# Optimization experiments

Hardware: AMD Instinct MI355X
Metric: run time of the kernel (lower is better)

## Reference

```python
import jax, jax.numpy as jnp
import numpy as np

K = 4  # Chebyshev order (layer._k)

def setup_inputs() -> dict:
    key = jax.random.key(0)
    k1, k2, k3, k4 = jax.random.split(key, 4)
    N, din, dout = 4096, 128, 128
    a = jax.random.normal(k1, (N, din), dtype=jnp.float32)            # layer input (only len used)
    r = jax.random.uniform(k2, (N, dout), dtype=jnp.float32)          # upstream relevance (positive)
    # sparse-ish binary directed adjacency, no self loops (avg degree ~16)
    adj = (jax.random.uniform(k3, (N, N)) < (16.0 / N)).astype(jnp.float32)
    adj = adj * (1.0 - jnp.eye(N, dtype=jnp.float32))
    W = jax.random.normal(k4, (dout, K * din), dtype=jnp.float32) * 0.05  # ChebConv linear weight [out, K*in]
    return {"a": a, "r": r, "adj": adj, "W": W}

def _forward(a, r, adj, W):
    N = a.shape[0]
    dW = W.shape[1] // K
    # Wk[k] = W[:, k*dW:(k+1)*dW].T  -> [K, dimY(in), dimJ(out)]; rho = abs
    rhoW = jnp.abs(jnp.stack([W[:, k * dW:(k + 1) * dW].T for k in range(K)]))
    # Laplacian: L = I - D^{-1/2} A D^{-1/2}, degrees clamped at 1 (in-degrees = column sums)
    dinv = jnp.clip(adj.sum(axis=0), 1.0, None) ** -0.5
    D = dinv[:, None] * adj * dinv[None, :]
    L = jnp.eye(N, dtype=adj.dtype) - D
    # Chebyshev polynomials T_0=I, T_1=L, T_k = 2 L T_{k-1} - T_{k-2}  -> [K, N, N]
    Ts = [jnp.eye(N, dtype=L.dtype), L]
    for _ in range(2, K):
        Ts.append(2.0 * (L @ Ts[-1]) - Ts[-2])
    Ak = jnp.stack(Ts[:K])
    # U[i,j,x,y] = sum_k Ak[k,i,x] * rhoW[k,y,j]; never materialized.
    # denom[i,j] = U.sum(dim=(2,3)) = sum_k (sum_x Ak[k,i,x]) * (sum_y rhoW[k,y,j])
    denom = jnp.einsum('ki,kj->ij', Ak.sum(axis=2), rhoW.sum(axis=1))
    c = r / denom
    # out[x,y] = einsum('ijxy,ij->xy', U, c) = sum_k Ak[k].T @ c @ rhoW[k].T
    return jnp.einsum('kix,kyj,ij->xy', Ak, rhoW, c)

def reference(a, r, adj, W):
    return _forward(a, r, adj, W)
```

## Files before the change

### kernel.cpp

```cpp
#include <hip/hip_runtime.h>
#include <cstdint>
#include <cstddef>

#define N_NODES 4096
#define FEAT 128
#define KCH 4
#define NNZ_CAP (1 << 18)
#define TB 512
#define T2CAP 2048
#define RSTRIDE 96

__device__ __forceinline__ int panel_of(int p) {
    return p < 3456 ? (p / 384) : (p < 3776 ? 9 : 10);
}

__global__ __launch_bounds__(256) void k_adj(const float* __restrict__ adj,
                                             int* __restrict__ deg,
                                             int* __restrict__ rdeg,
                                             int* __restrict__ rcolF) {
    int row = (blockIdx.x * 256 + threadIdx.x) >> 6;
    int lane = threadIdx.x & 63;
    const float* rowp = adj + (size_t)row * N_NODES;
    int base = 0;
    for (int it = 0; it < 64; ++it) {
        int x = it * 64 + lane;
        bool nz = rowp[x] != 0.0f;
        unsigned long long m = __ballot(nz);
        if (nz) {
            int idx = base + __popcll(m & ((1ull << lane) - 1ull));
            if (idx < RSTRIDE) rcolF[row * RSTRIDE + idx] = x;
            atomicAdd(&deg[x], 1);
        }
        base += __popcll(m);
    }
    if (lane == 0) rdeg[row] = (base > RSTRIDE) ? RSTRIDE : base;
}

__global__ __launch_bounds__(1024) void k_scan(const int* __restrict__ deg,
                                               float* __restrict__ dinv,
                                               int* __restrict__ colptr,
                                               int* __restrict__ colcur) {
    __shared__ int part[1024];
    int t = threadIdx.x;
    int v[4]; int s = 0;
    for (int c = 0; c < 4; ++c) {
        int idx = t * 4 + c;
        int di = deg[idx];
        v[c] = di;
        s += di;
        float dc = fmaxf((float)di, 1.0f);
        dinv[idx] = (float)(1.0 / sqrt((double)dc));
    }
    part[t] = s;
    __syncthreads();
    for (int off = 1; off < 1024; off <<= 1) {
        int add = (t >= off) ? part[t - off] : 0;
        __syncthreads();
        part[t] += add;
        __syncthreads();
    }
    int base = (t == 0) ? 0 : part[t - 1];
    for (int c = 0; c < 4; ++c) {
        int idx = t * 4 + c;
        colptr[idx] = base; colcur[idx] = base;
        base += v[c];
    }
    if (t == 1023) colptr[N_NODES] = base;
}

__global__ __launch_bounds__(256) void k_vals(const float* __restrict__ dinv,
                                              const int* __restrict__ rdeg,
                                              const int* __restrict__ rcolF,
                                              float* __restrict__ rlvalF,
                                              int* __restrict__ colcur,
                                              int* __restrict__ col_i,
                                              float* __restrict__ val) {
    int row = (blockIdx.x * 256 + threadIdx.x) >> 6;
    int lane = threadIdx.x & 63;
    int n = rdeg[row];
    float di = dinv[row];
    for (int e = lane; e < n; e += 64) {
        int x = rcolF[row * RSTRIDE + e];
        float dv = di * dinv[x];
        rlvalF[row * RSTRIDE + e] = -dv;
        int ec = atomicAdd(&colcur[x], 1);
        if (ec < NNZ_CAP) { col_i[ec] = row; val[ec] = dv; }
    }
}

__global__ void k_sw(const float* __restrict__ W, float* __restrict__ sW) {
    int tid = blockIdx.x * blockDim.x + threadIdx.x;
    int k = tid >> 7, j = tid & 127;
    float s = 0.f;
    for (int y = 0; y < FEAT; ++y)
        s += fabsf(W[(size_t)j * (KCH * FEAT) + k * FEAT + y]);
    sW[k * FEAT + j] = s;
}

__device__ __forceinline__ float np_pairwise_4096(const float* __restrict__ row,
                                                  float* r256, float* leaf,
                                                  float* bc, int t) {
    if (t < 256) {
        int L = t >> 3, j = t & 7;
        const float* p = row + L * 128 + j;
        float a = p[0];
        #pragma unroll
        for (int q = 1; q < 16; ++q) a += p[8 * q];
        r256[t] = a;
    }
    __syncthreads();
    if (t < 32) {
        const float* rr = r256 + t * 8;
        leaf[t] = ((rr[0] + rr[1]) + (rr[2] + rr[3])) + ((rr[4] + rr[5]) + (rr[6] + rr[7]));
    }
    __syncthreads();
    if (t == 0) {
        float v[32];
        #pragma unroll
        for (int q = 0; q < 32; ++q) v[q] = leaf[q];
        #pragma unroll
        for (int w = 16; w >= 1; w >>= 1)
            #pragma unroll
            for (int q = 0; q < 16; ++q)
                if (q < w) v[q] = v[2 * q] + v[2 * q + 1];
        bc[0] = v[0];
    }
    __syncthreads();
    float res = bc[0];
    __syncthreads();
    return res;
}

__global__ __launch_bounds__(TB) void k_t2(const int* __restrict__ rdeg,
                                           const int* __restrict__ rcolF,
                                           const float* __restrict__ rlvalF,
                                           int2* __restrict__ t2sp,
                                           int* __restrict__ t2cnt,
                                           float* __restrict__ sA) {
    __shared__ float gp[N_NODES];
    __shared__ int   scol[2048];
    __shared__ float sval[2048];
    __shared__ int   pcol[64];
    __shared__ float pLip[64];
    __shared__ int   pbeg[64], plen[64], poff[65];
    __shared__ int   ssplit;
    __shared__ float r256[256], leaf[32], bc[1];
    __shared__ int   wtot[8], wbase[8];
    int t = threadIdx.x;
    int i = blockIdx.x;
    int rp = i * RSTRIDE;
    int ol = rdeg[i];
    int cnt = ol + 1;
    if (cnt > 64) cnt = 64;
    if (t == 0) ssplit = 0;
    __syncthreads();
    if (t < ol && rcolF[rp + t] < i) atomicAdd(&ssplit, 1);
    __syncthreads();
    int split = ssplit;
    if (t < cnt) {
        int col; float lip;
        if (t < split)       { col = rcolF[rp + t];     lip = rlvalF[rp + t]; }
        else if (t == split) { col = i;                 lip = 1.0f; }
        else                 { col = rcolF[rp + t - 1]; lip = rlvalF[rp + t - 1]; }
        pcol[t] = col; pLip[t] = lip;
        pbeg[t] = col * RSTRIDE;
        plen[t] = rdeg[col] + 1;
    }
    float4* gp4 = (float4*)gp;
    const float4 z4 = make_float4(0.f, 0.f, 0.f, 0.f);
    #pragma unroll
    for (int u = 0; u < 2; ++u) gp4[t + u * TB] = z4;
    __syncthreads();
    if (t == 0) {
        int o = 0;
        for (int q = 0; q < cnt; ++q) { poff[q] = o; o += plen[q]; }
        poff[cnt] = o;
    }
    __syncthreads();
    int E = poff[cnt]; if (E > 2048) E = 2048;
    for (int idx = t; idx < E; idx += TB) {
        int lo = 0, hi = cnt - 1;
        while (lo < hi) { int mid = (lo + hi + 1) >> 1; if (poff[mid] <= idx) lo = mid; else hi = mid - 1; }
        int e = idx - poff[lo];
        if (e == plen[lo] - 1) { scol[idx] = pcol[lo]; sval[idx] = 1.0f; }
        else                   { scol[idx] = rcolF[pbeg[lo] + e]; sval[idx] = rlvalF[pbeg[lo] + e]; }
    }
    __syncthreads();
    int q0 = split;
    for (int e = t; e < plen[q0]; e += TB) { int idx = poff[q0] + e; gp[scol[idx]] = sval[idx]; }
    __syncthreads();
    float s1 = np_pairwise_4096(gp, r256, leaf, bc, t);
    for (int e = t; e < plen[q0]; e += TB) gp[scol[poff[q0] + e]] = 0.0f;
    __syncthreads();
    float tot[8];
    #pragma unroll
    for (int u = 0; u < 8; ++u) tot[u] = 0.0f;
    int q = 0;
    while (q < cnt) {
        int pid = panel_of(pcol[q]);
        while (q < cnt && panel_of(pcol[q]) == pid) {
            float lv = pLip[q];
            int o = poff[q], Lq = plen[q];
            for (int e = t; e < Lq; e += TB) {
                int idx = o + e; int x = scol[idx];
                gp[x] = fmaf(lv, sval[idx], gp[x]);
            }
            __syncthreads();
            ++q;
        }
        #pragma unroll
        for (int u2 = 0; u2 < 2; ++u2) {
            int idx = t + u2 * TB;
            float4 b = gp4[idx];
            tot[4 * u2 + 0] = tot[4 * u2 + 0] + b.x;
            tot[4 * u2 + 1] = tot[4 * u2 + 1] + b.y;
            tot[4 * u2 + 2] = tot[4 * u2 + 2] + b.z;
            tot[4 * u2 + 3] = tot[4 * u2 + 3] + b.w;
            gp4[idx] = z4;
        }
        __syncthreads();
    }
    #pragma unroll
    for (int u2 = 0; u2 < 2; ++u2) {
        int xb = 4 * t + 2048 * u2;
        float4 v;
        v.x = 2.0f * tot[4 * u2 + 0] - (xb + 0 == i ? 1.0f : 0.0f);
        v.y = 2.0f * tot[4 * u2 + 1] - (xb + 1 == i ? 1.0f : 0.0f);
        v.z = 2.0f * tot[4 * u2 + 2] - (xb + 2 == i ? 1.0f : 0.0f);
        v.w = 2.0f * tot[4 * u2 + 3] - (xb + 3 == i ? 1.0f : 0.0f);
        gp4[t + u2 * TB] = v;
    }
    __syncthreads();
    float s2 = np_pairwise_4096(gp, r256, leaf, bc, t);
    float4 ea = gp4[2 * t], eb = gp4[2 * t + 1];
    float ev[8] = {ea.x, ea.y, ea.z, ea.w, eb.x, eb.y, eb.z, eb.w};
    int cl = 0;
    #pragma unroll
    for (int u = 0; u < 8; ++u) cl += (ev[u] != 0.0f);
    int lane = t & 63, wv = t >> 6;
    int sc = cl;
    for (int off = 1; off < 64; off <<= 1) {
        int n = __shfl_up(sc, off);
        if (lane >= off) sc += n;
    }
    if (lane == 63) wtot[wv] = sc;
    __syncthreads();
    if (t == 0) {
        int b = 0;
        for (int wq = 0; wq < 8; ++wq) { wbase[wq] = b; b += wtot[wq]; }
        t2cnt[i] = (b > T2CAP) ? T2CAP : b;
    }
    __syncthreads();
    int pos = wbase[wv] + sc - cl;
    int2* dst = t2sp + (size_t)i * T2CAP;
    #pragma unroll
    for (int u = 0; u < 8; ++u) {
        if (ev[u] != 0.0f) {
            if (pos < T2CAP) dst[pos] = make_int2(t * 8 + u, __float_as_int(ev[u]));
            ++pos;
        }
    }
    if (t == 0) {
        sA[0 * N_NODES + i] = 1.0f;
        sA[1 * N_NODES + i] = s1;
        sA[2 * N_NODES + i] = s2;
    }
}

__global__ __launch_bounds__(TB) void k_t3(const int* __restrict__ rdeg,
                                           const int* __restrict__ rcolF,
                                           const float* __restrict__ rlvalF,
                                           const int2* __restrict__ t2sp,
                                           const int* __restrict__ t2cnt,
                                           float* __restrict__ sA) {
    __shared__ float gp[N_NODES];
    __shared__ int   pcol[64];
    __shared__ float pLip[64];
    __shared__ int   ssplit;
    __shared__ float r256[256], leaf[32], bc[1];
    int t = threadIdx.x;
    int i = blockIdx.x;
    int rp = i * RSTRIDE;
    int ol = rdeg[i];
    int cnt = ol + 1;
    if (cnt > 64) cnt = 64;
    if (t == 0) ssplit = 0;
    __syncthreads();
    if (t < ol && rcolF[rp + t] < i) atomicAdd(&ssplit, 1);
    __syncthreads();
    int split = ssplit;
    if (t < cnt) {
        if (t < split)       { pcol[t] = rcolF[rp + t];     pLip[t] = rlvalF[rp + t]; }
        else if (t == split) { pcol[t] = i;                  pLip[t] = 1.0f; }
        else                 { pcol[t] = rcolF[rp + t - 1];  pLip[t] = rlvalF[rp + t - 1]; }
    }
    float4* gp4 = (float4*)gp;
    const float4 z4 = make_float4(0.f, 0.f, 0.f, 0.f);
    #pragma unroll
    for (int u2 = 0; u2 < 2; ++u2) gp4[t + u2 * TB] = z4;
    __syncthreads();
    float tot[8];
    #pragma unroll
    for (int u = 0; u < 8; ++u) tot[u] = 0.0f;
    int q = 0;
    while (q < cnt) {
        int pid = panel_of(pcol[q]);
        while (q < cnt && panel_of(pcol[q]) == pid) {
            float lv = pLip[q];
            int p = pcol[q];
            int nn = t2cnt[p];
            const int2* sp = t2sp + (size_t)p * T2CAP;
            for (int e = t; e < nn; e += TB) {
                int2 en = sp[e];
                gp[en.x] = fmaf(lv, __int_as_float(en.y), gp[en.x]);
            }
            __syncthreads();
            ++q;
        }
        #pragma unroll
        for (int u2 = 0; u2 < 2; ++u2) {
            int idx = t + u2 * TB;
            float4 b = gp4[idx];
            tot[4 * u2 + 0] = tot[4 * u2 + 0] + b.x;
            tot[4 * u2 + 1] = tot[4 * u2 + 1] + b.y;
            tot[4 * u2 + 2] = tot[4 * u2 + 2] + b.z;
            tot[4 * u2 + 3] = tot[4 * u2 + 3] + b.w;
            gp4[idx] = z4;
        }
        __syncthreads();
    }
    #pragma unroll
    for (int u2 = 0; u2 < 2; ++u2) {
        float4 v;
        v.x = 2.0f * tot[4 * u2 + 0];
        v.y = 2.0f * tot[4 * u2 + 1];
        v.z = 2.0f * tot[4 * u2 + 2];
        v.w = 2.0f * tot[4 * u2 + 3];
        gp4[t + u2 * TB] = v;
    }
    __syncthreads();
    for (int e = t; e < ol; e += TB) { int x = rcolF[rp + e]; gp[x] = gp[x] - rlvalF[rp + e]; }
    if (t == 0) gp[i] = gp[i] - 1.0f;
    __syncthreads();
    float s3 = np_pairwise_4096(gp, r256, leaf, bc, t);
    if (t == 0) sA[3 * N_NODES + i] = s3;
}

__global__ __launch_bounds__(256) void k_cm(const float* __restrict__ r,
                                            const float* __restrict__ sA,
                                            const float* __restrict__ sW,
                                            const float* __restrict__ W,
                                            float* __restrict__ M) {
#pragma clang fp contract(off)
    __shared__ float cl[32][FEAT];
    int k = blockIdx.y;
    int ib = blockIdx.x * 32;
    int tx = threadIdx.x;
    int y = tx & 127, half = tx >> 7;
    for (int m = tx; m < 32 * FEAT; m += 256) {
        int i = ib + (m >> 7), j = m & 127;
        float denom = 0.0f;
        #pragma unroll
        for (int k2 = 0; k2 < KCH; ++k2) {
            float p = sA[k2 * N_NODES + i] * sW[k2 * FEAT + j];
            denom = denom + p;
        }
        cl[m >> 7][m & 127] = r[(size_t)i * FEAT + j] / denom;
    }
    __syncthreads();
    float acc[16];
    #pragma unroll
    for (int u = 0; u < 16; ++u) acc[u] = 0.0f;
    for (int j = 0; j < FEAT; ++j) {
        float a = fabsf(W[(size_t)j * (KCH * FEAT) + k * FEAT + y]);
        #pragma unroll
        for (int u = 0; u < 16; ++u) acc[u] += a * cl[half * 16 + u][j];
    }
    #pragma unroll
    for (int u = 0; u < 16; ++u)
        M[(size_t)k * N_NODES * FEAT + (size_t)(ib + half * 16 + u) * FEAT + y] = acc[u];
}

__global__ void k_h1(const int* __restrict__ colptr, const int* __restrict__ col_i,
                     const float* __restrict__ val, const float* __restrict__ M,
                     float* __restrict__ B2) {
    int x = blockIdx.x * 2 + (threadIdx.x >> 7);
    int y = threadIdx.x & 127;
    const float* M2 = M + (size_t)2 * N_NODES * FEAT;
    const float* M3 = M + (size_t)3 * N_NODES * FEAT;
    int e0 = colptr[x], e1 = colptr[x + 1];
    if (e1 > NNZ_CAP) e1 = NNZ_CAP;
    float g = 0.0f;
    for (int e = e0; e < e1; ++e)
        g += val[e] * M3[(size_t)col_i[e] * FEAT + y];
    size_t o = (size_t)x * FEAT + y;
    B2[o] = 2.0f * M2[o] + 4.0f * (M3[o] - g);
}

__global__ void k_h2(const int* __restrict__ colptr, const int* __restrict__ col_i,
                     const float* __restrict__ val, const float* __restrict__ M,
                     const float* __restrict__ B2, float* __restrict__ B3) {
    int x = blockIdx.x * 2 + (threadIdx.x >> 7);
    int y = threadIdx.x & 127;
    const float* M1 = M + (size_t)N_NODES * FEAT;
    const float* M3 = M + (size_t)3 * N_NODES * FEAT;
    int e0 = colptr[x], e1 = colptr[x + 1];
    if (e1 > NNZ_CAP) e1 = NNZ_CAP;
    float g = 0.0f;
    for (int e = e0; e < e1; ++e)
        g += val[e] * B2[(size_t)col_i[e] * FEAT + y];
    size_t o = (size_t)x * FEAT + y;
    B3[o] = (M1[o] - 3.0f * M3[o]) + (B2[o] - g);
}

__global__ void k_h3(const int* __restrict__ colptr, const int* __restrict__ col_i,
                     const float* __restrict__ val, const float* __restrict__ M,
                     const float* __restrict__ B3, float* __restrict__ out) {
    int x = blockIdx.x * 2 + (threadIdx.x >> 7);
    int y = threadIdx.x & 127;
    const float* M0 = M;
    const float* M2 = M + (size_t)2 * N_NODES * FEAT;
    int e0 = colptr[x], e1 = colptr[x + 1];
    if (e1 > NNZ_CAP) e1 = NNZ_CAP;
    float g = 0.0f;
    for (int e = e0; e < e1; ++e)
        g += val[e] * B3[(size_t)col_i[e] * FEAT + y];
    size_t o = (size_t)x * FEAT + y;
    out[o] = (M0[o] - M2[o]) + (B3[o] - g);
}

extern "C" void kernel_launch(void* const* d_in, const int* in_sizes, int n_in,
                              void* d_out, int out_size, void* d_ws, size_t ws_size,
                              hipStream_t stream) {
    const float* r   = (const float*)d_in[1];
    const float* adj = (const float*)d_in[2];
    const float* W   = (const float*)d_in[3];
    float* out = (float*)d_out;

    char* w = (char*)d_ws;
    auto take = [&](size_t bytes) {
        char* p = w;
        w += (bytes + 255) & ~(size_t)255;
        return p;
    };
    int*   deg    = (int*)take((size_t)N_NODES * 4);
    int*   rdeg   = (int*)take((size_t)N_NODES * 4);
    float* dinv   = (float*)take((size_t)N_NODES * 4);
    int*   colcur = (int*)take((size_t)N_NODES * 4);
    int*   colptr = (int*)take((size_t)(N_NODES + 1) * 4);
    int*   col_i  = (int*)take((size_t)NNZ_CAP * 4);
    float* val    = (float*)take((size_t)NNZ_CAP * 4);
    int*   rcolF  = (int*)take((size_t)N_NODES * RSTRIDE * 4);
    float* rlvalF = (float*)take((size_t)N_NODES * RSTRIDE * 4);
    float* sW     = (float*)take((size_t)KCH * FEAT * 4);
    float* sA     = (float*)take((size_t)KCH * N_NODES * 4);
    float* M      = (float*)take((size_t)KCH * N_NODES * FEAT * 4);
    float* B2     = (float*)take((size_t)N_NODES * FEAT * 4);
    float* B3     = (float*)take((size_t)N_NODES * FEAT * 4);
    int*   t2cnt  = (int*)take((size_t)N_NODES * 4);
    int2*  t2sp   = (int2*)take((size_t)N_NODES * T2CAP * 8);

    hipMemsetAsync(deg, 0, (size_t)N_NODES * 4, stream);
    k_adj<<<N_NODES / 4, 256, 0, stream>>>(adj, deg, rdeg, rcolF);
    k_scan<<<1, 1024, 0, stream>>>(deg, dinv, colptr, colcur);
    k_vals<<<N_NODES / 4, 256, 0, stream>>>(dinv, rdeg, rcolF, rlvalF,
                                            colcur, col_i, val);
    k_sw<<<2, 256, 0, stream>>>(W, sW);
    k_t2<<<N_NODES, TB, 0, stream>>>(rdeg, rcolF, rlvalF, t2sp, t2cnt, sA);
    k_t3<<<N_NODES, TB, 0, stream>>>(rdeg, rcolF, rlvalF, t2sp, t2cnt, sA);
    k_cm<<<dim3(N_NODES / 32, KCH), 256, 0, stream>>>(r, sA, sW, W, M);
    k_h1<<<N_NODES / 2, 256, 0, stream>>>(colptr, col_i, val, M, B2);
    k_h2<<<N_NODES / 2, 256, 0, stream>>>(colptr, col_i, val, M, B2, B3);
    k_h3<<<N_NODES / 2, 256, 0, stream>>>(colptr, col_i, val, M, B3, out);
}
```

Measured before the change: 373.2 us.

## Stage T2 rows in LDS for k_t3, use wave-shuffle scan, and shrink k_cm tiles

k_t3 now loads the sparse T2 entries of several neighbour rows from global memory into shared memory in batches, storing each column as a ushort and each value as a float. It then scatters from the staged copy, with the t2cnt loads hoisted into a per-row table. k_scan replaces the 1024-thread Hillis-Steele scan, which needed two barriers per step, with a wave-level shuffle scan plus a serial sum over the 16 wave totals. k_cm halves its row tile to 16 so it launches twice as many blocks, each holding fewer accumulators. Staging adds about 12KB of LDS per k_t3 block, which may reduce occupancy, and the extra barriers per chunk could offset the benefit of batching the global loads.

```diff
diff --git a/kernel.cpp b/kernel.cpp
--- a/kernel.cpp
+++ b/kernel.cpp
@@ -40,8 +40,10 @@
                                                float* __restrict__ dinv,
                                                int* __restrict__ colptr,
                                                int* __restrict__ colcur) {
-    __shared__ int part[1024];
+    __shared__ int wsum[16];
+    __shared__ int wbase[16];
     int t = threadIdx.x;
+    int lane = t & 63, wv = t >> 6;
     int v[4]; int s = 0;
     for (int c = 0; c < 4; ++c) {
         int idx = t * 4 + c;
@@ -51,15 +53,19 @@
         float dc = fmaxf((float)di, 1.0f);
         dinv[idx] = (float)(1.0 / sqrt((double)dc));
     }
-    part[t] = s;
-    __syncthreads();
-    for (int off = 1; off < 1024; off <<= 1) {
-        int add = (t >= off) ? part[t - off] : 0;
-        __syncthreads();
-        part[t] += add;
-        __syncthreads();
-    }
-    int base = (t == 0) ? 0 : part[t - 1];
+    int sc = s;
+    for (int off = 1; off < 64; off <<= 1) {
+        int n = __shfl_up(sc, off);
+        if (lane >= off) sc += n;
+    }
+    if (lane == 63) wsum[wv] = sc;
+    __syncthreads();
+    if (t == 0) {
+        int b = 0;
+        for (int q2 = 0; q2 < 16; ++q2) { wbase[q2] = b; b += wsum[q2]; }
+    }
+    __syncthreads();
+    int base = wbase[wv] + sc - s;
     for (int c = 0; c < 4; ++c) {
         int idx = t * 4 + c;
         colptr[idx] = base; colcur[idx] = base;
@@ -274,9 +280,13 @@
                                            const int* __restrict__ t2cnt,
                                            float* __restrict__ sA) {
     __shared__ float gp[N_NODES];
+    __shared__ unsigned short stc[2048];
+    __shared__ float stv[2048];
     __shared__ int   pcol[64];
     __shared__ float pLip[64];
-    __shared__ int   ssplit;
+    __shared__ int   pnn[64];
+    __shared__ int   sqoff[64];
+    __shared__ int   ssplit, schunk;
     __shared__ float r256[256], leaf[32], bc[1];
     int t = threadIdx.x;
     int i = blockIdx.x;
@@ -290,9 +300,11 @@
     __syncthreads();
     int split = ssplit;
     if (t < cnt) {
-        if (t < split)       { pcol[t] = rcolF[rp + t];     pLip[t] = rlvalF[rp + t]; }
-        else if (t == split) { pcol[t] = i;                  pLip[t] = 1.0f; }
-        else                 { pcol[t] = rcolF[rp + t - 1];  pLip[t] = rlvalF[rp + t - 1]; }
+        int col; float lip;
+        if (t < split)       { col = rcolF[rp + t];     lip = rlvalF[rp + t]; }
+        else if (t == split) { col = i;                  lip = 1.0f; }
+        else                 { col = rcolF[rp + t - 1];  lip = rlvalF[rp + t - 1]; }
+        pcol[t] = col; pLip[t] = lip; pnn[t] = t2cnt[col];
     }
     float4* gp4 = (float4*)gp;
     const float4 z4 = make_float4(0.f, 0.f, 0.f, 0.f);
@@ -303,31 +315,50 @@
     #pragma unroll
     for (int u = 0; u < 8; ++u) tot[u] = 0.0f;
     int q = 0;
+    int stqe = 0;
     while (q < cnt) {
-        int pid = panel_of(pcol[q]);
-        while (q < cnt && panel_of(pcol[q]) == pid) {
-            float lv = pLip[q];
-            int p = pcol[q];
-            int nn = t2cnt[p];
-            const int2* sp = t2sp + (size_t)p * T2CAP;
-            for (int e = t; e < nn; e += TB) {
-                int2 en = sp[e];
-                gp[en.x] = fmaf(lv, __int_as_float(en.y), gp[en.x]);
+        if (q >= stqe) {
+            if (t == 0) {
+                int o = 0; int qq = q;
+                while (qq < cnt && o + pnn[qq] <= 2048) { sqoff[qq] = o; o += pnn[qq]; ++qq; }
+                schunk = qq;
             }
             __syncthreads();
-            ++q;
-        }
-        #pragma unroll
-        for (int u2 = 0; u2 < 2; ++u2) {
-            int idx = t + u2 * TB;
-            float4 b = gp4[idx];
-            tot[4 * u2 + 0] = tot[4 * u2 + 0] + b.x;
-            tot[4 * u2 + 1] = tot[4 * u2 + 1] + b.y;
-            tot[4 * u2 + 2] = tot[4 * u2 + 2] + b.z;
-            tot[4 * u2 + 3] = tot[4 * u2 + 3] + b.w;
-            gp4[idx] = z4;
-        }
-        __syncthreads();
+            stqe = schunk;
+            for (int qq = q; qq < stqe; ++qq) {
+                int p = pcol[qq], nn = pnn[qq], o = sqoff[qq];
+                const int2* sp = t2sp + (size_t)p * T2CAP;
+                for (int e = t; e < nn; e += TB) {
+                    int2 en = sp[e];
+                    stc[o + e] = (unsigned short)en.x;
+                    stv[o + e] = __int_as_float(en.y);
+                }
+            }
+            __syncthreads();
+        }
+        {
+            float lv = pLip[q];
+            int nn = pnn[q], o = sqoff[q];
+            for (int e = t; e < nn; e += TB) {
+                int x = stc[o + e];
+                gp[x] = fmaf(lv, stv[o + e], gp[x]);
+            }
+            __syncthreads();
+        }
+        ++q;
+        if (q == cnt || panel_of(pcol[q]) != panel_of(pcol[q - 1])) {
+            #pragma unroll
+            for (int u2 = 0; u2 < 2; ++u2) {
+                int idx = t + u2 * TB;
+                float4 b = gp4[idx];
+                tot[4 * u2 + 0] = tot[4 * u2 + 0] + b.x;
+                tot[4 * u2 + 1] = tot[4 * u2 + 1] + b.y;
+                tot[4 * u2 + 2] = tot[4 * u2 + 2] + b.z;
+                tot[4 * u2 + 3] = tot[4 * u2 + 3] + b.w;
+                gp4[idx] = z4;
+            }
+            __syncthreads();
+        }
     }
     #pragma unroll
     for (int u2 = 0; u2 < 2; ++u2) {
@@ -352,12 +383,12 @@
                                             const float* __restrict__ W,
                                             float* __restrict__ M) {
 #pragma clang fp contract(off)
-    __shared__ float cl[32][FEAT];
+    __shared__ float cl[16][FEAT];
     int k = blockIdx.y;
-    int ib = blockIdx.x * 32;
+    int ib = blockIdx.x * 16;
     int tx = threadIdx.x;
     int y = tx & 127, half = tx >> 7;
-    for (int m = tx; m < 32 * FEAT; m += 256) {
+    for (int m = tx; m < 16 * FEAT; m += 256) {
         int i = ib + (m >> 7), j = m & 127;
         float denom = 0.0f;
         #pragma unroll
@@ -368,17 +399,17 @@
         cl[m >> 7][m & 127] = r[(size_t)i * FEAT + j] / denom;
     }
     __syncthreads();
-    float acc[16];
-    #pragma unroll
-    for (int u = 0; u < 16; ++u) acc[u] = 0.0f;
+    float acc[8];
+    #pragma unroll
+    for (int u = 0; u < 8; ++u) acc[u] = 0.0f;
     for (int j = 0; j < FEAT; ++j) {
         float a = fabsf(W[(size_t)j * (KCH * FEAT) + k * FEAT + y]);
         #pragma unroll
-        for (int u = 0; u < 16; ++u) acc[u] += a * cl[half * 16 + u][j];
-    }
-    #pragma unroll
-    for (int u = 0; u < 16; ++u)
-        M[(size_t)k * N_NODES * FEAT + (size_t)(ib + half * 16 + u) * FEAT + y] = acc[u];
+        for (int u = 0; u < 8; ++u) acc[u] += a * cl[half * 8 + u][j];
+    }
+    #pragma unroll
+    for (int u = 0; u < 8; ++u)
+        M[(size_t)k * N_NODES * FEAT + (size_t)(ib + half * 8 + u) * FEAT + y] = acc[u];
 }
 
 __global__ void k_h1(const int* __restrict__ colptr, const int* __restrict__ col_i,
@@ -468,7 +499,7 @@
     k_sw<<<2, 256, 0, stream>>>(W, sW);
     k_t2<<<N_NODES, TB, 0, stream>>>(rdeg, rcolF, rlvalF, t2sp, t2cnt, sA);
     k_t3<<<N_NODES, TB, 0, stream>>>(rdeg, rcolF, rlvalF, t2sp, t2cnt, sA);
-    k_cm<<<dim3(N_NODES / 32, KCH), 256, 0, stream>>>(r, sA, sW, W, M);
+    k_cm<<<dim3(N_NODES / 16, KCH), 256, 0, stream>>>(r, sA, sW, W, M);
     k_h1<<<N_NODES / 2, 256, 0, stream>>>(colptr, col_i, val, M, B2);
     k_h2<<<N_NODES / 2, 256, 0, stream>>>(colptr, col_i, val, M, B2, B3);
     k_h3<<<N_NODES / 2, 256, 0, stream>>>(colptr, col_i, val, M, B3, out);
```

Measured after the change: 393.8 us. +5.5%, slower.
